# Kernel tuning notes

Hardware: AMD Instinct MI355X
Metric: run time of the kernel (lower is better)

Reference implementation:

```python
import jax, jax.numpy as jnp
import numpy as np

INPUT_SIZE = 64
HIDDEN = 64
BATCH = 1024
SEQ = 512


def _uniform(key, shape, k):
    return jax.random.uniform(key, shape, dtype=jnp.float32, minval=-k, maxval=k)


def setup_inputs() -> dict:
    key = jax.random.key(0)
    ks = jax.random.split(key, 12)
    k = 1.0 / np.sqrt(HIDDEN)
    x = jax.random.normal(ks[0], (BATCH, SEQ, INPUT_SIZE), dtype=jnp.float32)
    # PyTorch nn.LSTM params, gate order (i, f, g, o), layout [4H, in]
    w_ih0 = _uniform(ks[1], (4 * HIDDEN, INPUT_SIZE), k)
    w_hh0 = _uniform(ks[2], (4 * HIDDEN, HIDDEN), k)
    b_ih0 = _uniform(ks[3], (4 * HIDDEN,), k)
    b_hh0 = _uniform(ks[4], (4 * HIDDEN,), k)
    w_ih1 = _uniform(ks[5], (4 * HIDDEN, HIDDEN), k)
    w_hh1 = _uniform(ks[6], (4 * HIDDEN, HIDDEN), k)
    b_ih1 = _uniform(ks[7], (4 * HIDDEN,), k)
    b_hh1 = _uniform(ks[8], (4 * HIDDEN,), k)
    fc_w = _uniform(ks[9], (1, HIDDEN), k)
    fc_b = _uniform(ks[10], (1,), k)
    return {"x": x, "w_ih0": w_ih0, "w_hh0": w_hh0, "b_ih0": b_ih0, "b_hh0": b_hh0,
            "w_ih1": w_ih1, "w_hh1": w_hh1, "b_ih1": b_ih1, "b_hh1": b_hh1,
            "fc_w": fc_w, "fc_b": fc_b}


def _lstm_layer(x, w_ih, w_hh, b_ih, b_hh):
    # x: [B, T, D] -> h sequence [B, T, H]; PyTorch gate order i, f, g, o
    B = x.shape[0]
    H = w_hh.shape[1]
    # precompute input contribution for all timesteps (big GEMM)
    pre = jnp.einsum('btd,gd->btg', x, w_ih) + b_ih + b_hh  # [B, T, 4H]

    def step(carry, p_t):
        h, c = carry
        g = p_t + h @ w_hh.T  # [B, 4H]
        i, f, gg, o = jnp.split(g, 4, axis=-1)
        i = jax.nn.sigmoid(i)
        f = jax.nn.sigmoid(f)
        gg = jnp.tanh(gg)
        o = jax.nn.sigmoid(o)
        c = f * c + i * gg
        h = o * jnp.tanh(c)
        return (h, c), h

    h0 = jnp.zeros((B, H), x.dtype)
    (_, _), hs = jax.lax.scan(step, (h0, h0), jnp.swapaxes(pre, 0, 1))  # hs: [T, B, H]
    return jnp.swapaxes(hs, 0, 1)


def reference(x, w_ih0, w_hh0, b_ih0, b_hh0, w_ih1, w_hh1, b_ih1, b_hh1, fc_w, fc_b):
    h1 = _lstm_layer(x, w_ih0, w_hh0, b_ih0, b_hh0)   # [B, T, H]
    h2 = _lstm_layer(h1, w_ih1, w_hh1, b_ih1, b_hh1)  # [B, T, H] (dropout inactive in eval)
    last = h2[:, -1, :]                               # [B, H]
    return (last @ fc_w.T + fc_b).reshape(-1)         # [B]
```

## Files before the change

kernel.cpp:

```cpp
#include <hip/hip_runtime.h>

#define TSEQ 512

typedef _Float16 half8 __attribute__((ext_vector_type(8)));
typedef __attribute__((ext_vector_type(4))) float f32x4;

#define MFMAH(a,b,c) __builtin_amdgcn_mfma_f32_16x16x32_f16(a,b,c,0,0,0)

static __device__ __forceinline__ float sigm(float x){ return __builtin_amdgcn_rcpf(1.0f + __expf(-x)); }
static __device__ __forceinline__ float tanh_f(float x){ return 1.0f - 2.0f*__builtin_amdgcn_rcpf(__expf(2.0f*x)+1.0f); }

static __device__ __forceinline__ short f2h(float v){
  union { _Float16 h; short s; } u; u.h = (_Float16)v; return u.s;
}

static __device__ __forceinline__ void lds_drain(){
  __builtin_amdgcn_s_waitcnt(0xC07F);
  __asm__ __volatile__("" ::: "memory");
}

extern "C" __global__ void __launch_bounds__(512, 2)
lstm_h16c(const float* __restrict__ x,
          const float* __restrict__ wih0, const float* __restrict__ whh0,
          const float* __restrict__ bih0, const float* __restrict__ bhh0,
          const float* __restrict__ wih1, const float* __restrict__ whh1,
          const float* __restrict__ bih1, const float* __restrict__ bhh1,
          const float* __restrict__ fcw,  const float* __restrict__ fcb,
          float* __restrict__ out)
{
  __shared__ __align__(16) short act[6][256];
  __shared__ __align__(16) float gbuf[2][1024];
  __shared__ float fcpart[16];

  const int tid = threadIdx.x;
  const int wv  = tid >> 6;
  const int gm  = wv >> 2;
  const int p   = wv & 3;
  const int ln  = tid & 63;
  const int lq  = ln >> 4;
  const int lr  = ln & 15;
  const int b0  = blockIdx.x << 2;
  const int jc  = (p << 4) + lr;
  const int si  = (((jc>>5)*4 + ((jc>>3)&3))*4 + lq)*8 + (jc&7);
  const int foff = lq*32 + lr*8;
  float* const gme = &gbuf[gm][0];
  const bool wlane = (lq == 0);

  half8 W[2][2][4];
  {
    const float* w_op[2] = { gm ? wih1 : wih0, gm ? whh1 : whh0 };
#pragma unroll
    for (int op = 0; op < 2; ++op)
#pragma unroll
      for (int F = 0; F < 2; ++F)
#pragma unroll
        for (int q = 0; q < 4; ++q){
          const float* src = w_op[op] + ((q<<6) + jc)*64 + F*32 + lq*8;
#pragma unroll
          for (int e = 0; e < 8; ++e)
            W[op][F][q][e] = (_Float16)src[e];
        }
  }
  f32x4 Bq[4];
  {
    const float* bi = gm ? bih1 : bih0;
    const float* bh = gm ? bhh1 : bhh0;
#pragma unroll
    for (int q = 0; q < 4; ++q){
      float b = bi[(q<<6)+jc] + bh[(q<<6)+jc];
      Bq[q][0] = b; Bq[q][1] = b; Bq[q][2] = b; Bq[q][3] = b;
    }
  }

  const float* xq = x + (size_t)(b0 + lq)*(TSEQ*64) + jc;

  float cst = 0.f, hval = 0.f, xv = 0.f;
  half8 aF[4];
#pragma unroll
  for (int f = 0; f < 4; ++f) aF[f] = (half8){0,0,0,0,0,0,0,0};

  for (int idx = tid; idx < 2*256; idx += 512) act[4 + (idx>>8)][idx & 255] = 0;
  if (gm == 0){
    act[0][si] = f2h(xq[0]);
    act[1][si] = f2h(xq[64]);
    xv = xq[128];
  }
  __syncthreads();

  if (gm == 0){
    if (lr < 4){
      aF[0] = *(const half8*)(&act[0][0] + foff);
      aF[1] = *(const half8*)(&act[0][0] + foff + 128);
    }
    f32x4 acc[4];
#pragma unroll
    for (int q = 0; q < 4; ++q){
      acc[q] = MFMAH(aF[0], W[0][0][q], Bq[q]);
      acc[q] = MFMAH(aF[1], W[0][1][q], acc[q]);
    }
    if (wlane){
#pragma unroll
      for (int q = 0; q < 4; ++q) *(f32x4*)&gme[q*256 + jc*4] = acc[q];
    }
    lds_drain();
    float gi = sigm  (gme[0*256 + jc*4 + lq]);
    float gf = sigm  (gme[1*256 + jc*4 + lq]);
    float gg = tanh_f(gme[2*256 + jc*4 + lq]);
    float go = sigm  (gme[3*256 + jc*4 + lq]);
    cst  = gf*cst + gi*gg;
    hval = go * tanh_f(cst);
    act[2][si] = f2h(hval);
  }
  __syncthreads();

  if (gm == 1){
#pragma unroll 2
    for (int i = 0; i < TSEQ; ++i){
      const int cb = i & 1, nb = cb ^ 1;
      if (lr < 4){
        aF[0] = *(const half8*)(&act[2+cb][0] + foff);
        aF[1] = *(const half8*)(&act[2+cb][0] + foff + 128);
        aF[2] = *(const half8*)(&act[4+nb][0] + foff);
        aF[3] = *(const half8*)(&act[4+nb][0] + foff + 128);
      }
      f32x4 acc[4];
#pragma unroll
      for (int q = 0; q < 4; ++q){
        acc[q] = MFMAH(aF[0], W[0][0][q], Bq[q]);
        acc[q] = MFMAH(aF[1], W[0][1][q], acc[q]);
        acc[q] = MFMAH(aF[2], W[1][0][q], acc[q]);
        acc[q] = MFMAH(aF[3], W[1][1][q], acc[q]);
      }
      if (wlane){
#pragma unroll
        for (int q = 0; q < 4; ++q) *(f32x4*)&gme[q*256 + jc*4] = acc[q];
      }
      lds_drain();
      float gi = sigm  (gme[0*256 + jc*4 + lq]);
      float gf = sigm  (gme[1*256 + jc*4 + lq]);
      float gg = tanh_f(gme[2*256 + jc*4 + lq]);
      float go = sigm  (gme[3*256 + jc*4 + lq]);
      cst  = gf*cst + gi*gg;
      hval = go * tanh_f(cst);
      act[4+cb][si] = f2h(hval);
      __syncthreads();
    }
  } else {
#pragma unroll 2
    for (int i = 0; i < TSEQ; ++i){
      const int cb = i & 1, nb = cb ^ 1;
      if (i < TSEQ-1){
        if (lr < 4){
          aF[0] = *(const half8*)(&act[0+nb][0] + foff);
          aF[1] = *(const half8*)(&act[0+nb][0] + foff + 128);
          aF[2] = *(const half8*)(&act[2+cb][0] + foff);
          aF[3] = *(const half8*)(&act[2+cb][0] + foff + 128);
        }
        f32x4 acc[4];
#pragma unroll
        for (int q = 0; q < 4; ++q){
          acc[q] = MFMAH(aF[0], W[0][0][q], Bq[q]);
          acc[q] = MFMAH(aF[1], W[0][1][q], acc[q]);
          acc[q] = MFMAH(aF[2], W[1][0][q], acc[q]);
          acc[q] = MFMAH(aF[3], W[1][1][q], acc[q]);
        }
        if (wlane){
#pragma unroll
          for (int q = 0; q < 4; ++q) *(f32x4*)&gme[q*256 + jc*4] = acc[q];
        }
        lds_drain();
        float gi = sigm  (gme[0*256 + jc*4 + lq]);
        float gf = sigm  (gme[1*256 + jc*4 + lq]);
        float gg = tanh_f(gme[2*256 + jc*4 + lq]);
        float go = sigm  (gme[3*256 + jc*4 + lq]);
        cst  = gf*cst + gi*gg;
        hval = go * tanh_f(cst);
        act[2+nb][si] = f2h(hval);
        if (i < TSEQ-2) act[0+cb][si] = f2h(xv);
        int tn = i + 3; if (tn > TSEQ-1) tn = TSEQ-1;
        xv = xq[tn << 6];
      }
      __syncthreads();
    }
  }

  if (gm == 1){
    float v = hval * fcw[jc];
    v += __shfl_xor(v, 1); v += __shfl_xor(v, 2);
    v += __shfl_xor(v, 4); v += __shfl_xor(v, 8);
    if (lr == 0) fcpart[p*4 + lq] = v;
  }
  __syncthreads();
  if (tid < 4)
    out[b0 + tid] = fcpart[tid] + fcpart[4+tid] + fcpart[8+tid] + fcpart[12+tid] + fcb[0];
}

extern "C" void kernel_launch(void* const* d_in, const int* in_sizes, int n_in,
                              void* d_out, int out_size, void* d_ws, size_t ws_size,
                              hipStream_t stream) {
  const float* x    = (const float*)d_in[0];
  const float* wih0 = (const float*)d_in[1];
  const float* whh0 = (const float*)d_in[2];
  const float* bih0 = (const float*)d_in[3];
  const float* bhh0 = (const float*)d_in[4];
  const float* wih1 = (const float*)d_in[5];
  const float* whh1 = (const float*)d_in[6];
  const float* bih1 = (const float*)d_in[7];
  const float* bhh1 = (const float*)d_in[8];
  const float* fcw  = (const float*)d_in[9];
  const float* fcb  = (const float*)d_in[10];
  float* out = (float*)d_out;

  hipLaunchKernelGGL(lstm_h16c, dim3(256), dim3(512), 0, stream,
                     x, wih0, whh0, bih0, bhh0, wih1, whh1, bih1, bhh1, fcw, fcb, out);
}
```

Before: 454.8 us.

## Swap MFMA operands so gate outputs land in registers, removing LDS gate round-trip

Weights become the A operand and activations the B operand of the MFMA, so each lane holds four gate pre-activations for its own batch row in accumulator registers. This removes the per-step store of gates to LDS, the drain and the reload, and each lane now updates four hidden units instead of one. The activation buffers are padded rows (stride 72) written as short4 vectors, and __syncthreads is replaced by a raw s_barrier plus explicit LDS drain. The cost is more transcendental work per lane and MFMA lanes computing on batch columns that are padding (16 columns, only 4 batches).

```diff
diff --git a/kernel.cpp b/kernel.cpp
--- a/kernel.cpp
+++ b/kernel.cpp
@@ -4,6 +4,7 @@
 
 typedef _Float16 half8 __attribute__((ext_vector_type(8)));
 typedef __attribute__((ext_vector_type(4))) float f32x4;
+typedef short short4v __attribute__((ext_vector_type(4)));
 
 #define MFMAH(a,b,c) __builtin_amdgcn_mfma_f32_16x16x32_f16(a,b,c,0,0,0)
 
@@ -19,17 +20,24 @@
   __asm__ __volatile__("" ::: "memory");
 }
 
+static __device__ __forceinline__ void bar(){
+  __asm__ __volatile__("" ::: "memory");
+  __builtin_amdgcn_s_barrier();
+  __asm__ __volatile__("" ::: "memory");
+}
+
+#define SROW 72
+
 extern "C" __global__ void __launch_bounds__(512, 2)
-lstm_h16c(const float* __restrict__ x,
-          const float* __restrict__ wih0, const float* __restrict__ whh0,
-          const float* __restrict__ bih0, const float* __restrict__ bhh0,
-          const float* __restrict__ wih1, const float* __restrict__ whh1,
-          const float* __restrict__ bih1, const float* __restrict__ bhh1,
-          const float* __restrict__ fcw,  const float* __restrict__ fcb,
-          float* __restrict__ out)
+lstm_swp(const float* __restrict__ x,
+         const float* __restrict__ wih0, const float* __restrict__ whh0,
+         const float* __restrict__ bih0, const float* __restrict__ bhh0,
+         const float* __restrict__ wih1, const float* __restrict__ whh1,
+         const float* __restrict__ bih1, const float* __restrict__ bhh1,
+         const float* __restrict__ fcw,  const float* __restrict__ fcb,
+         float* __restrict__ out)
 {
-  __shared__ __align__(16) short act[6][256];
-  __shared__ __align__(16) float gbuf[2][1024];
+  __shared__ __align__(16) short act[6][16*SROW];
   __shared__ float fcpart[16];
 
   const int tid = threadIdx.x;
@@ -40,11 +48,10 @@
   const int lq  = ln >> 4;
   const int lr  = ln & 15;
   const int b0  = blockIdx.x << 2;
-  const int jc  = (p << 4) + lr;
-  const int si  = (((jc>>5)*4 + ((jc>>3)&3))*4 + lq)*8 + (jc&7);
-  const int foff = lq*32 + lr*8;
-  float* const gme = &gbuf[gm][0];
-  const bool wlane = (lq == 0);
+  const int wrow = (p << 4) + lr;
+  const int boff = lr*SROW + (lq << 3);
+  const int hwoff = lr*SROW + (p << 4) + (lq << 2);
+  const int soff  = lq*SROW + (p << 4) + lr;
 
   half8 W[2][2][4];
   {
@@ -55,7 +62,7 @@
       for (int F = 0; F < 2; ++F)
 #pragma unroll
         for (int q = 0; q < 4; ++q){
-          const float* src = w_op[op] + ((q<<6) + jc)*64 + F*32 + lq*8;
+          const float* src = w_op[op] + ((q<<6) + wrow)*64 + F*32 + lq*8;
 #pragma unroll
           for (int e = 0; e < 8; ++e)
             W[op][F][q][e] = (_Float16)src[e];
@@ -65,51 +72,53 @@
   {
     const float* bi = gm ? bih1 : bih0;
     const float* bh = gm ? bhh1 : bhh0;
+    const int ub = (p<<4) + (lq<<2);
+#pragma unroll
+    for (int q = 0; q < 4; ++q)
+#pragma unroll
+      for (int m = 0; m < 4; ++m)
+        Bq[q][m] = bi[(q<<6)+ub+m] + bh[(q<<6)+ub+m];
+  }
+
+  const float* xq = x + (size_t)(b0 + lq)*(TSEQ*64) + (p<<4) + lr;
+
+  float c0=0.f, c1=0.f, c2=0.f, c3=0.f;
+  float hf0=0.f, hf1=0.f, hf2=0.f, hf3=0.f;
+  float xv = 0.f;
+
+  {
+    int* a32 = (int*)&act[0][0];
+    for (int idx = tid; idx < 6*16*SROW/2; idx += 512) a32[idx] = 0;
+  }
+  __syncthreads();
+  if (gm == 0){
+    act[0][soff] = f2h(xq[0]);
+    act[1][soff] = f2h(xq[64]);
+    xv = xq[128];
+  }
+  __syncthreads();
+
+  if (gm == 0){
+    const short* xb = &act[0][0];
+    half8 bx0 = *(const half8*)(xb + boff);
+    half8 bx1 = *(const half8*)(xb + boff + 32);
+    f32x4 acc[4];
 #pragma unroll
     for (int q = 0; q < 4; ++q){
-      float b = bi[(q<<6)+jc] + bh[(q<<6)+jc];
-      Bq[q][0] = b; Bq[q][1] = b; Bq[q][2] = b; Bq[q][3] = b;
+      acc[q] = MFMAH(W[0][0][q], bx0, Bq[q]);
+      acc[q] = MFMAH(W[0][1][q], bx1, acc[q]);
     }
-  }
-
-  const float* xq = x + (size_t)(b0 + lq)*(TSEQ*64) + jc;
-
-  float cst = 0.f, hval = 0.f, xv = 0.f;
-  half8 aF[4];
-#pragma unroll
-  for (int f = 0; f < 4; ++f) aF[f] = (half8){0,0,0,0,0,0,0,0};
-
-  for (int idx = tid; idx < 2*256; idx += 512) act[4 + (idx>>8)][idx & 255] = 0;
-  if (gm == 0){
-    act[0][si] = f2h(xq[0]);
-    act[1][si] = f2h(xq[64]);
-    xv = xq[128];
-  }
-  __syncthreads();
-
-  if (gm == 0){
-    if (lr < 4){
-      aF[0] = *(const half8*)(&act[0][0] + foff);
-      aF[1] = *(const half8*)(&act[0][0] + foff + 128);
-    }
-    f32x4 acc[4];
-#pragma unroll
-    for (int q = 0; q < 4; ++q){
-      acc[q] = MFMAH(aF[0], W[0][0][q], Bq[q]);
-      acc[q] = MFMAH(aF[1], W[0][1][q], acc[q]);
-    }
-    if (wlane){
-#pragma unroll
-      for (int q = 0; q < 4; ++q) *(f32x4*)&gme[q*256 + jc*4] = acc[q];
-    }
-    lds_drain();
-    float gi = sigm  (gme[0*256 + jc*4 + lq]);
-    float gf = sigm  (gme[1*256 + jc*4 + lq]);
-    float gg = tanh_f(gme[2*256 + jc*4 + lq]);
-    float go = sigm  (gme[3*256 + jc*4 + lq]);
-    cst  = gf*cst + gi*gg;
-    hval = go * tanh_f(cst);
-    act[2][si] = f2h(hval);
+    float gi, gf, gg, go;
+    gi=sigm(acc[0][0]); gf=sigm(acc[1][0]); gg=tanh_f(acc[2][0]); go=sigm(acc[3][0]);
+    c0 = gf*c0 + gi*gg; hf0 = go*tanh_f(c0);
+    gi=sigm(acc[0][1]); gf=sigm(acc[1][1]); gg=tanh_f(acc[2][1]); go=sigm(acc[3][1]);
+    c1 = gf*c1 + gi*gg; hf1 = go*tanh_f(c1);
+    gi=sigm(acc[0][2]); gf=sigm(acc[1][2]); gg=tanh_f(acc[2][2]); go=sigm(acc[3][2]);
+    c2 = gf*c2 + gi*gg; hf2 = go*tanh_f(c2);
+    gi=sigm(acc[0][3]); gf=sigm(acc[1][3]); gg=tanh_f(acc[2][3]); go=sigm(acc[3][3]);
+    c3 = gf*c3 + gi*gg; hf3 = go*tanh_f(c3);
+    short4v hv = { f2h(hf0), f2h(hf1), f2h(hf2), f2h(hf3) };
+    *(short4v*)(&act[2][0] + hwoff) = hv;
   }
   __syncthreads();
 
@@ -117,78 +126,79 @@
 #pragma unroll 2
     for (int i = 0; i < TSEQ; ++i){
       const int cb = i & 1, nb = cb ^ 1;
-      if (lr < 4){
-        aF[0] = *(const half8*)(&act[2+cb][0] + foff);
-        aF[1] = *(const half8*)(&act[2+cb][0] + foff + 128);
-        aF[2] = *(const half8*)(&act[4+nb][0] + foff);
-        aF[3] = *(const half8*)(&act[4+nb][0] + foff + 128);
+      const short* h0b = &act[2+cb][0];
+      const short* h1b = &act[4+nb][0];
+      half8 ba0 = *(const half8*)(h0b + boff);
+      half8 bb0 = *(const half8*)(h1b + boff);
+      half8 ba1 = *(const half8*)(h0b + boff + 32);
+      half8 bb1 = *(const half8*)(h1b + boff + 32);
+      f32x4 acc[4];
+#pragma unroll
+      for (int q = 0; q < 4; ++q){
+        acc[q] = MFMAH(W[0][0][q], ba0, Bq[q]);
+        acc[q] = MFMAH(W[1][0][q], bb0, acc[q]);
+        acc[q] = MFMAH(W[0][1][q], ba1, acc[q]);
+        acc[q] = MFMAH(W[1][1][q], bb1, acc[q]);
       }
-      f32x4 acc[4];
-#pragma unroll
-      for (int q = 0; q < 4; ++q){
-        acc[q] = MFMAH(aF[0], W[0][0][q], Bq[q]);
-        acc[q] = MFMAH(aF[1], W[0][1][q], acc[q]);
-        acc[q] = MFMAH(aF[2], W[1][0][q], acc[q]);
-        acc[q] = MFMAH(aF[3], W[1][1][q], acc[q]);
-      }
-      if (wlane){
-#pragma unroll
-        for (int q = 0; q < 4; ++q) *(f32x4*)&gme[q*256 + jc*4] = acc[q];
-      }
+      float gi, gf, gg, go;
+      gi=sigm(acc[0][0]); gf=sigm(acc[1][0]); gg=tanh_f(acc[2][0]); go=sigm(acc[3][0]);
+      c0 = gf*c0 + gi*gg; hf0 = go*tanh_f(c0);
+      gi=sigm(acc[0][1]); gf=sigm(acc[1][1]); gg=tanh_f(acc[2][1]); go=sigm(acc[3][1]);
+      c1 = gf*c1 + gi*gg; hf1 = go*tanh_f(c1);
+      gi=sigm(acc[0][2]); gf=sigm(acc[1][2]); gg=tanh_f(acc[2][2]); go=sigm(acc[3][2]);
+      c2 = gf*c2 + gi*gg; hf2 = go*tanh_f(c2);
+      gi=sigm(acc[0][3]); gf=sigm(acc[1][3]); gg=tanh_f(acc[2][3]); go=sigm(acc[3][3]);
+      c3 = gf*c3 + gi*gg; hf3 = go*tanh_f(c3);
+      short4v hv = { f2h(hf0), f2h(hf1), f2h(hf2), f2h(hf3) };
+      *(short4v*)(&act[4+cb][0] + hwoff) = hv;
       lds_drain();
-      float gi = sigm  (gme[0*256 + jc*4 + lq]);
-      float gf = sigm  (gme[1*256 + jc*4 + lq]);
-      float gg = tanh_f(gme[2*256 + jc*4 + lq]);
-      float go = sigm  (gme[3*256 + jc*4 + lq]);
-      cst  = gf*cst + gi*gg;
-      hval = go * tanh_f(cst);
-      act[4+cb][si] = f2h(hval);
-      __syncthreads();
+      bar();
     }
   } else {
 #pragma unroll 2
     for (int i = 0; i < TSEQ; ++i){
       const int cb = i & 1, nb = cb ^ 1;
       if (i < TSEQ-1){
-        if (lr < 4){
-          aF[0] = *(const half8*)(&act[0+nb][0] + foff);
-          aF[1] = *(const half8*)(&act[0+nb][0] + foff + 128);
-          aF[2] = *(const half8*)(&act[2+cb][0] + foff);
-          aF[3] = *(const half8*)(&act[2+cb][0] + foff + 128);
+        const short* xb  = &act[0+nb][0];
+        const short* h0b = &act[2+cb][0];
+        half8 ba0 = *(const half8*)(xb  + boff);
+        half8 bb0 = *(const half8*)(h0b + boff);
+        half8 ba1 = *(const half8*)(xb  + boff + 32);
+        half8 bb1 = *(const half8*)(h0b + boff + 32);
+        f32x4 acc[4];
+#pragma unroll
+        for (int q = 0; q < 4; ++q){
+          acc[q] = MFMAH(W[0][0][q], ba0, Bq[q]);
+          acc[q] = MFMAH(W[1][0][q], bb0, acc[q]);
+          acc[q] = MFMAH(W[0][1][q], ba1, acc[q]);
+          acc[q] = MFMAH(W[1][1][q], bb1, acc[q]);
         }
-        f32x4 acc[4];
-#pragma unroll
-        for (int q = 0; q < 4; ++q){
-          acc[q] = MFMAH(aF[0], W[0][0][q], Bq[q]);
-          acc[q] = MFMAH(aF[1], W[0][1][q], acc[q]);
-          acc[q] = MFMAH(aF[2], W[1][0][q], acc[q]);
-          acc[q] = MFMAH(aF[3], W[1][1][q], acc[q]);
-        }
-        if (wlane){
-#pragma unroll
-          for (int q = 0; q < 4; ++q) *(f32x4*)&gme[q*256 + jc*4] = acc[q];
-        }
-        lds_drain();
-        float gi = sigm  (gme[0*256 + jc*4 + lq]);
-        float gf = sigm  (gme[1*256 + jc*4 + lq]);
-        float gg = tanh_f(gme[2*256 + jc*4 + lq]);
-        float go = sigm  (gme[3*256 + jc*4 + lq]);
-        cst  = gf*cst + gi*gg;
-        hval = go * tanh_f(cst);
-        act[2+nb][si] = f2h(hval);
-        if (i < TSEQ-2) act[0+cb][si] = f2h(xv);
+        float gi, gf, gg, go;
+        gi=sigm(acc[0][0]); gf=sigm(acc[1][0]); gg=tanh_f(acc[2][0]); go=sigm(acc[3][0]);
+        c0 = gf*c0 + gi*gg; hf0 = go*tanh_f(c0);
+        gi=sigm(acc[0][1]); gf=sigm(acc[1][1]); gg=tanh_f(acc[2][1]); go=sigm(acc[3][1]);
+        c1 = gf*c1 + gi*gg; hf1 = go*tanh_f(c1);
+        gi=sigm(acc[0][2]); gf=sigm(acc[1][2]); gg=tanh_f(acc[2][2]); go=sigm(acc[3][2]);
+        c2 = gf*c2 + gi*gg; hf2 = go*tanh_f(c2);
+        gi=sigm(acc[0][3]); gf=sigm(acc[1][3]); gg=tanh_f(acc[2][3]); go=sigm(acc[3][3]);
+        c3 = gf*c3 + gi*gg; hf3 = go*tanh_f(c3);
+        short4v hv = { f2h(hf0), f2h(hf1), f2h(hf2), f2h(hf3) };
+        *(short4v*)(&act[2+nb][0] + hwoff) = hv;
+        if (i < TSEQ-2) act[0+cb][soff] = f2h(xv);
         int tn = i + 3; if (tn > TSEQ-1) tn = TSEQ-1;
         xv = xq[tn << 6];
       }
-      __syncthreads();
+      lds_drain();
+      bar();
     }
   }
 
   if (gm == 1){
-    float v = hval * fcw[jc];
-    v += __shfl_xor(v, 1); v += __shfl_xor(v, 2);
-    v += __shfl_xor(v, 4); v += __shfl_xor(v, 8);
-    if (lr == 0) fcpart[p*4 + lq] = v;
+    const f32x4 fw = *(const f32x4*)(fcw + (p<<4) + (lq<<2));
+    float v = hf0*fw[0] + hf1*fw[1] + hf2*fw[2] + hf3*fw[3];
+    v += __shfl_xor(v, 16);
+    v += __shfl_xor(v, 32);
+    if (lq == 0 && lr < 4) fcpart[p*4 + lr] = v;
   }
   __syncthreads();
   if (tid < 4)
@@ -211,6 +221,6 @@
   const float* fcb  = (const float*)d_in[10];
   float* out = (float*)d_out;
 
-  hipLaunchKernelGGL(lstm_h16c, dim3(256), dim3(512), 0, stream,
+  hipLaunchKernelGGL(lstm_swp, dim3(256), dim3(512), 0, stream,
                      x, wih0, whh0, bih0, bhh0, wih1, whh1, bih1, bhh1, fcw, fcb, out);
 }
```

Result: slower. 531.5 us (+16.9%).
